# Kernel optimization log

Hardware: AMD Instinct MI355X
Metric: run time of the kernel (lower is better)

The kernel has to match this reference:

```python
import jax, jax.numpy as jnp
import numpy as np

D_MODEL = 1024
NUM_HEADS = 16
HEAD_DIM = D_MODEL // NUM_HEADS


def setup_inputs() -> dict:
    key = jax.random.key(0)
    ks = jax.random.split(key, 5)
    B, S, D_IN = 2, 2048, 1024
    x = jax.random.normal(ks[0], (B, S, D_IN), dtype=jnp.float32)
    std = 0.02
    wq = jax.random.normal(ks[1], (D_MODEL, D_IN), dtype=jnp.float32) * std
    wk = jax.random.normal(ks[2], (D_MODEL, D_IN), dtype=jnp.float32) * std
    wv = jax.random.normal(ks[3], (D_MODEL, D_IN), dtype=jnp.float32) * std
    wo = jax.random.normal(ks[4], (D_IN, D_MODEL), dtype=jnp.float32) * std
    return {"x": x, "wq": wq, "wk": wk, "wv": wv, "wo": wo}


def _mha(x, wq, wk, wv, wo):
    B, S, _ = x.shape
    H, Dh = NUM_HEADS, HEAD_DIM
    # projections: Linear applies x @ W.T with W of shape [out, in]
    q = (x @ wq.T).reshape(B, S, H, Dh).transpose(0, 2, 1, 3)  # [B,H,S,Dh]
    k = (x @ wk.T).reshape(B, S, H, Dh).transpose(0, 2, 1, 3)
    v = (x @ wv.T).reshape(B, S, H, Dh).transpose(0, 2, 1, 3)
    scores = jnp.einsum('bhqd,bhkd->bhqk', q, k) / jnp.sqrt(jnp.float32(Dh))
    causal = jnp.tril(jnp.ones((S, S), dtype=bool))  # True where attended
    scores = jnp.where(causal, scores, -jnp.inf)
    attn = jax.nn.softmax(scores, axis=-1)
    out = jnp.einsum('bhqk,bhkd->bhqd', attn, v)  # [B,H,S,Dh]
    out = out.transpose(0, 2, 1, 3).reshape(B, S, H * Dh)
    return out @ wo.T


def reference(x, wq, wk, wv, wo):
    return _mha(x, wq, wk, wv, wo)
```

## Files before the change

### kernel.cpp

```cpp
#include <hip/hip_runtime.h>
#include <hip/hip_bf16.h>
#include <stdint.h>

using bf16 = __hip_bfloat16;
typedef __attribute__((ext_vector_type(4))) short shorts4;
typedef __attribute__((ext_vector_type(8))) short short8;
typedef __attribute__((ext_vector_type(4))) float floatx4;
typedef __attribute__((ext_vector_type(16))) float floatx16;
typedef __attribute__((ext_vector_type(4))) unsigned int uintx4;

constexpr int BATCH = 2;
constexpr int SEQ   = 2048;
constexpr int NH    = 16;
constexpr int DH    = 64;
constexpr int DM    = 1024;
constexpr int MROWS = BATCH * SEQ;
constexpr int OUTN  = MROWS * DM;
constexpr int WN    = DM * DM;

__device__ inline short bfbits(float x) {
    bf16 h = __float2bfloat16(x);
    return __builtin_bit_cast(short, h);
}

__device__ inline unsigned pack2(float a, float b) {
    return (unsigned)(unsigned short)bfbits(a) |
           ((unsigned)(unsigned short)bfbits(b) << 16);
}

__device__ inline void async16(bf16* lds, const bf16* g) {
    __builtin_amdgcn_global_load_lds(
        (const __attribute__((address_space(1))) unsigned int*)g,
        (__attribute__((address_space(3))) unsigned int*)lds, 16, 0, 0);
}

__device__ inline void cvt8(const float* src, bf16* dst) {
    float4 f0 = *(const float4*)(src);
    float4 f1 = *(const float4*)(src + 4);
    short8 o;
    o[0] = bfbits(f0.x); o[1] = bfbits(f0.y); o[2] = bfbits(f0.z); o[3] = bfbits(f0.w);
    o[4] = bfbits(f1.x); o[5] = bfbits(f1.y); o[6] = bfbits(f1.z); o[7] = bfbits(f1.w);
    *(short8*)(dst) = o;
}

__global__ __launch_bounds__(256)
void cvt_all(const float* __restrict__ x,  const float* __restrict__ wq,
             const float* __restrict__ wk, const float* __restrict__ wv,
             const float* __restrict__ wo, bf16* __restrict__ dst,
             bf16* __restrict__ wob)
{
    const size_t i = ((size_t)blockIdx.x * 256 + threadIdx.x) * 8;
    if (i < (size_t)OUTN + 3 * WN) {
        const float* src; size_t off;
        if (i < (size_t)OUTN)               { src = x;  off = i; }
        else if (i < (size_t)OUTN + WN)     { src = wq; off = i - OUTN; }
        else if (i < (size_t)OUTN + 2 * WN) { src = wk; off = i - OUTN - WN; }
        else                                { src = wv; off = i - OUTN - 2 * (size_t)WN; }
        cvt8(src + off, dst + i);
    } else {
        const size_t off = i - OUTN - 3 * (size_t)WN;
        cvt8(wo + off, wob + off);
    }
}

__global__ __launch_bounds__(256)
void cvt_inputs(const float* __restrict__ x,  const float* __restrict__ wq,
                const float* __restrict__ wk, const float* __restrict__ wv,
                bf16* __restrict__ dst)
{
    const size_t i = ((size_t)blockIdx.x * 256 + threadIdx.x) * 8;
    const float* src; size_t off;
    if (i < (size_t)OUTN)               { src = x;  off = i; }
    else if (i < (size_t)OUTN + WN)     { src = wq; off = i - OUTN; }
    else if (i < (size_t)OUTN + 2 * WN) { src = wk; off = i - OUTN - WN; }
    else                                { src = wv; off = i - OUTN - 2 * (size_t)WN; }
    cvt8(src + off, dst + i);
}

__global__ __launch_bounds__(256)
void cvt_wo(const float* __restrict__ wo, bf16* __restrict__ dst)
{
    const size_t i = ((size_t)blockIdx.x * 256 + threadIdx.x) * 8;
    cvt8(wo + i, dst + i);
}

template<int MODE, int NZ>
__global__ __launch_bounds__(512, 2)
void gemm_mfma(const bf16* __restrict__ A,
               const bf16* __restrict__ W0, const bf16* __restrict__ W1,
               const bf16* __restrict__ W2,
               bf16* __restrict__ C0, bf16* __restrict__ C1, bf16* __restrict__ C2,
               float* __restrict__ F)
{
    __shared__ __align__(16) bf16 smem[(1 + NZ) * 8192 * 2];

    const int t    = threadIdx.x;
    const int wave = t >> 6;
    const int lane = t & 63;
    const int quad = lane >> 4;
    const int l16  = lane & 15;
    const int m0 = blockIdx.y * 128;
    const int n0 = blockIdx.x * 128;
    const int wr = (wave >> 2) * 64;
    const int wc = (wave & 3) * 32;

    const bf16* Wp[3] = {W0, W1, W2};

    floatx4 acc[NZ][4][2] = {};

    auto stage = [&](int kt, int bb) {
        bf16* Bb = smem + bb * (1 + NZ) * 8192;
        const int k0 = kt * 64;
        #pragma unroll
        for (int p = 0; p < 2; p++) {
            const int ck = p * 512 + t;
            const int kr = ck >> 3;
            const int kg = (ck & 7) ^ (kr & 7);
            async16(Bb + ck * 8, A + (size_t)(m0 + kr) * DM + k0 + kg * 8);
            #pragma unroll
            for (int zz = 0; zz < NZ; zz++)
                async16(Bb + (1 + zz) * 8192 + ck * 8,
                        Wp[zz] + (size_t)(n0 + kr) * DM + k0 + kg * 8);
        }
    };

    stage(0, 0);
    __syncthreads();

    for (int kt = 0; kt < DM / 64; ++kt) {
        const int cur = kt & 1;
        if (kt + 1 < DM / 64) stage(kt + 1, cur ^ 1);

        const bf16* Bb = smem + cur * (1 + NZ) * 8192;

        #pragma unroll
        for (int ks = 0; ks < 2; ks++) {
            short8 af[4];
            #pragma unroll
            for (int i = 0; i < 4; i++) {
                const int r = wr + i * 16 + l16;
                af[i] = *(const short8*)(Bb + r * 64 + ((ks * 4 + quad) ^ (r & 7)) * 8);
            }
            #pragma unroll
            for (int zz = 0; zz < NZ; zz++) {
                short8 wf[2];
                #pragma unroll
                for (int j = 0; j < 2; j++) {
                    const int n = wc + j * 16 + l16;
                    wf[j] = *(const short8*)(Bb + (1 + zz) * 8192 + n * 64 +
                                             ((ks * 4 + quad) ^ (n & 7)) * 8);
                }
                __builtin_amdgcn_s_setprio(1);
                #pragma unroll
                for (int i = 0; i < 4; i++)
                    #pragma unroll
                    for (int j = 0; j < 2; j++)
                        acc[zz][i][j] = __builtin_amdgcn_mfma_f32_16x16x32_bf16(
                            af[i], wf[j], acc[zz][i][j], 0, 0, 0);
                __builtin_amdgcn_s_setprio(0);
            }
        }
        __syncthreads();
    }

    #pragma unroll
    for (int zz = 0; zz < NZ; zz++) {
        #pragma unroll
        for (int i = 0; i < 4; i++) {
            #pragma unroll
            for (int j = 0; j < 2; j++) {
                if (MODE == 0 && zz == 2) {
                    const int s0 = m0 + wr + i * 16 + quad * 4;
                    const int gn = n0 + wc + j * 16 + l16;
                    const int b = s0 >> 11, sr = s0 & (SEQ - 1);
                    const int h = gn >> 6,  d = gn & (DH - 1);
                    shorts4 pv;
                    #pragma unroll
                    for (int r = 0; r < 4; r++) pv[r] = bfbits(acc[zz][i][j][r]);
                    *(shorts4*)(C2 + (((size_t)(b * NH + h)) * DH + d) * SEQ + sr) = pv;
                } else {
                    #pragma unroll
                    for (int r = 0; r < 4; r++) {
                        const int gm = m0 + wr + i * 16 + quad * 4 + r;
                        const int gn = n0 + wc + j * 16 + l16;
                        if (MODE == 1) {
                            F[(size_t)gm * DM + gn] = acc[zz][i][j][r];
                        } else {
                            float av = acc[zz][i][j][r];
                            if (zz == 0) av *= 0.18033688f;
                            bf16* dst = (zz == 0) ? C0 : C1;
                            dst[(size_t)gm * DM + gn] = __float2bfloat16(av);
                        }
                    }
                }
            }
        }
    }
}

__device__ __forceinline__ void attn_tile(const bf16* Ks, int kbase, int qrow,
                                          const short8 (&qf)[4],
                                          floatx16 (&oacc)[2], float& lsum,
                                          int khalf, int hi, int l32)
{
    if (kbase > qrow + 31) return;
    const bf16* Vs = Ks + 8192;
    const int qg = qrow + l32;

    #pragma unroll
    for (int kt = 0; kt < 2; kt++) {
        const int kb = kbase + kt * 32;
        if (kb > qrow + 31) continue;

        const int krow = khalf * 64 + kt * 32 + l32;
        floatx16 sc = {};
        #pragma unroll
        for (int sg = 0; sg < 4; sg++) {
            const int g = (sg * 2 + hi) ^ (krow & 7);
            short8 kf = *(const short8*)(Ks + krow * 64 + g * 8);
            sc = __builtin_amdgcn_mfma_f32_32x32x16_bf16(kf, qf[sg], sc, 0, 0, 0);
        }

        if (kb + 31 > qrow) {
            #pragma unroll
            for (int r = 0; r < 16; r++) {
                const int key = kb + (r & 3) + 8 * (r >> 2) + 4 * hi;
                sc[r] = (key <= qg) ? sc[r] : -1e30f;
            }
        }

        #pragma unroll
        for (int r = 0; r < 16; r++) {
            const float p = __builtin_amdgcn_exp2f(sc[r]);
            sc[r] = p;
            lsum += p;
        }

        unsigned d[4][2];
        #pragma unroll
        for (int g = 0; g < 4; g++) {
            d[g][0] = pack2(sc[4 * g + 0], sc[4 * g + 1]);
            d[g][1] = pack2(sc[4 * g + 2], sc[4 * g + 3]);
        }

        #pragma unroll
        for (int h16 = 0; h16 < 2; h16++) {
            const unsigned a0 = d[h16 * 2][0],     a1 = d[h16 * 2][1];
            const unsigned b0 = d[h16 * 2 + 1][0], b1 = d[h16 * 2 + 1][1];
            const unsigned mine0 = hi ? b0 : a0, mine1 = hi ? b1 : a1;
            const unsigned give0 = hi ? a0 : b0, give1 = hi ? a1 : b1;
            const unsigned r0 = (unsigned)__shfl_xor((int)give0, 32, 64);
            const unsigned r1 = (unsigned)__shfl_xor((int)give1, 32, 64);
            uintx4 pw;
            pw[0] = hi ? r0 : mine0;
            pw[1] = hi ? r1 : mine1;
            pw[2] = hi ? mine0 : r0;
            pw[3] = hi ? mine1 : r1;
            short8 pb = __builtin_bit_cast(short8, pw);

            const int Gbase = khalf * 8 + kt * 4 + h16 * 2 + hi;
            #pragma unroll
            for (int tile = 0; tile < 2; tile++) {
                const int vrow = tile * 32 + l32;
                const int vg = Gbase ^ (vrow & 15);
                short8 vf = *(const short8*)(Vs + vrow * 128 + vg * 8);
                oacc[tile] = __builtin_amdgcn_mfma_f32_32x32x16_bf16(vf, pb, oacc[tile], 0, 0, 0);
            }
        }
    }
}

__global__ __launch_bounds__(512, 2)
void attn_flash(bf16* __restrict__ Q, const bf16* __restrict__ K,
                const bf16* __restrict__ Vt)
{
    __shared__ __align__(16) bf16 smem[49152];

    const int t    = threadIdx.x;
    const int wave = t >> 6;
    const int lane = t & 63;
    const int hi   = lane >> 5;
    const int l32  = lane & 31;

    const int id  = blockIdx.x + 8 * (blockIdx.y + NH * blockIdx.z);
    const int xcd = id & 7;
    const int jj  = id >> 3;
    const int p   = xcd * 4 + (jj >> 3);
    const int h   = p & (NH - 1);
    const int b   = p >> 4;
    const int qtA = jj & 7;
    const int qtB = 15 - qtA;

    const int hc  = h * DH;
    const size_t rowb = (size_t)b * SEQ;
    const size_t bhv  = ((size_t)(b * NH + h)) * SEQ * DH;

    const int qw    = wave & 3;
    const int khalf = wave >> 2;
    const int qrA = qtA * 128 + qw * 32;
    const int qrB = qtB * 128 + qw * 32;

    short8 qfA[4], qfB[4];
    #pragma unroll
    for (int sg = 0; sg < 4; sg++) {
        qfA[sg] = *(const short8*)(Q + (rowb + qrA + l32) * DM + hc + sg * 16 + hi * 8);
        qfB[sg] = *(const short8*)(Q + (rowb + qrB + l32) * DM + hc + sg * 16 + hi * 8);
    }

    floatx16 oaccA[2] = {}, oaccB[2] = {};
    float lsumA = 0.f, lsumB = 0.f;

    constexpr int NSLOT = 17;

    auto slotK0 = [&](int s) { return (s <= qtA ? s : s - qtA - 1) * 128; };

    auto stage = [&](int s) {
        bf16* Kb = smem + (s % 3) * 16384;
        bf16* Vb = Kb + 8192;
        const int k0 = slotK0(s);
        #pragma unroll
        for (int pp = 0; pp < 2; pp++) {
            const int ck = pp * 512 + t;
            const int kr = ck >> 3;
            const int kg = (ck & 7) ^ (kr & 7);
            async16(Kb + ck * 8, K + (rowb + k0 + kr) * DM + hc + kg * 8);
            const int vr = ck >> 4;
            const int vg = (ck & 15) ^ (vr & 15);
            async16(Vb + ck * 8, Vt + bhv + (size_t)vr * SEQ + k0 + vg * 8);
        }
    };

    stage(0);
    stage(1);
    for (int s = 0; s < NSLOT - 1; ++s) {
        asm volatile("s_waitcnt vmcnt(4)" ::: "memory");
        __builtin_amdgcn_s_barrier();
        if (s + 2 < NSLOT) stage(s + 2);
        const bf16* Ks = smem + (s % 3) * 16384;
        if (s <= qtA)
            attn_tile(Ks, s * 128 + khalf * 64, qrA, qfA, oaccA, lsumA, khalf, hi, l32);
        else
            attn_tile(Ks, (s - qtA - 1) * 128 + khalf * 64, qrB, qfB, oaccB, lsumB, khalf, hi, l32);
    }
    asm volatile("s_waitcnt vmcnt(0)" ::: "memory");
    __builtin_amdgcn_s_barrier();
    attn_tile(smem + ((NSLOT - 1) % 3) * 16384,
              (NSLOT - 2 - qtA) * 128 + khalf * 64, qrB, qfB, oaccB, lsumB, khalf, hi, l32);

    lsumA += __shfl_xor(lsumA, 32, 64);
    lsumB += __shfl_xor(lsumB, 32, 64);

    __syncthreads();
    float* dmp = (float*)smem;
    float* lP  = dmp + 2 * 4 * 32 * 66;
    if (khalf == 1) {
        #pragma unroll
        for (int m = 0; m < 2; m++) {
            const floatx16* oc = m ? oaccB : oaccA;
            #pragma unroll
            for (int tile = 0; tile < 2; tile++)
                #pragma unroll
                for (int r = 0; r < 16; r++) {
                    const int dd = tile * 32 + (r & 3) + 8 * (r >> 2) + 4 * hi;
                    dmp[((m * 4 + qw) * 32 + l32) * 66 + dd] = oc[tile][r];
                }
            if (!hi) lP[(m * 4 + qw) * 32 + l32] = m ? lsumB : lsumA;
        }
    }
    __syncthreads();

    if (khalf == 0) {
        bf16* T8 = smem + 34304 + qw * 2304;
        #pragma unroll
        for (int m = 0; m < 2; m++) {
            const floatx16* oc = m ? oaccB : oaccA;
            const float lt = (m ? lsumB : lsumA) + lP[(m * 4 + qw) * 32 + l32];
            const float invl = 1.0f / lt;
            const int qrow = m ? qrB : qrA;
            #pragma unroll
            for (int tile = 0; tile < 2; tile++)
                #pragma unroll
                for (int rq = 0; rq < 4; rq++) {
                    shorts4 v4;
                    #pragma unroll
                    for (int sg = 0; sg < 4; sg++) {
                        const int r = rq * 4 + sg;
                        const int dd = tile * 32 + (r & 3) + 8 * (r >> 2) + 4 * hi;
                        const float comb = oc[tile][r] + dmp[((m * 4 + qw) * 32 + l32) * 66 + dd];
                        v4[sg] = bfbits(comb * invl);
                    }
                    *(shorts4*)(T8 + l32 * 72 + tile * 32 + rq * 8 + hi * 4) = v4;
                }
            asm volatile("s_waitcnt lgkmcnt(0)" ::: "memory");
            #pragma unroll
            for (int p2 = 0; p2 < 4; p2++) {
                const int rq = (lane >> 3) + p2 * 8;
                const int dd = (lane & 7) * 8;
                short8 v8 = *(const short8*)(T8 + rq * 72 + dd);
                *(short8*)(Q + (rowb + qrow + rq) * DM + hc + dd) = v8;
            }
            asm volatile("s_waitcnt lgkmcnt(0)" ::: "memory");
        }
    }
}

extern "C" void kernel_launch(void* const* d_in, const int* in_sizes, int n_in,
                              void* d_out, int out_size, void* d_ws, size_t ws_size,
                              hipStream_t stream)
{
    const float* x  = (const float*)d_in[0];
    const float* wq = (const float*)d_in[1];
    const float* wk = (const float*)d_in[2];
    const float* wv = (const float*)d_in[3];
    const float* wo = (const float*)d_in[4];
    float* out = (float*)d_out;

    bf16* qb = (bf16*)d_ws;
    bf16* kb = qb + (size_t)OUTN;
    bf16* vb = kb + (size_t)OUTN;

    bf16* xb  = (bf16*)d_out;
    bf16* wqb = xb + (size_t)OUTN;
    bf16* wkb = wqb + WN;
    bf16* wvb = wkb + WN;

    const bool wsBig = ws_size >= (size_t)(3 * (size_t)OUTN + WN) * sizeof(bf16);

    if (wsBig) {
        bf16* wob = vb + (size_t)OUTN;
        cvt_all<<<(OUTN + 4 * WN) / (8 * 256), 256, 0, stream>>>(
            x, wq, wk, wv, wo, xb, wob);
        gemm_mfma<0, 3><<<dim3(DM / 128, MROWS / 128), dim3(512), 0, stream>>>(
            xb, wqb, wkb, wvb, qb, kb, vb, nullptr);
        attn_flash<<<dim3(8, NH, BATCH), dim3(512), 0, stream>>>(qb, kb, vb);
        gemm_mfma<1, 1><<<dim3(DM / 128, MROWS / 128), dim3(512), 0, stream>>>(
            qb, wob, nullptr, nullptr, nullptr, nullptr, nullptr, out);
    } else {
        cvt_inputs<<<(OUTN + 3 * WN) / (8 * 256), 256, 0, stream>>>(x, wq, wk, wv, xb);
        gemm_mfma<0, 3><<<dim3(DM / 128, MROWS / 128), dim3(512), 0, stream>>>(
            xb, wqb, wkb, wvb, qb, kb, vb, nullptr);
        attn_flash<<<dim3(8, NH, BATCH), dim3(512), 0, stream>>>(qb, kb, vb);
        bf16* wob = kb;
        cvt_wo<<<WN / (8 * 256), 256, 0, stream>>>(wo, wob);
        gemm_mfma<1, 1><<<dim3(DM / 128, MROWS / 128), dim3(512), 0, stream>>>(
            qb, wob, nullptr, nullptr, nullptr, nullptr, nullptr, out);
    }
}
```

Measured before the change: 157.5 us.

## Split attention key tile across four waves per query group with 1024-thread blocks

The attention kernel now runs 16 waves per block instead of 8. Each query group of 32 rows is served by four waves, and each wave handles one 32-key quarter of the 128-key tile instead of a 64-key half. Staging issues one K and one V chunk per thread, and the final combine reduces partial outputs and row sums from four waves through shared memory in four sync-separated passes. This aims to raise wave-level parallelism and latency hiding during the MFMA and exp work, at the cost of more block barriers, a longer reduction epilogue, and tighter register and occupancy limits with 1024 threads.

Result: slower. 210.2 us (+33.5%).

```diff
diff --git a/kernel.cpp b/kernel.cpp
--- a/kernel.cpp
+++ b/kernel.cpp
@@ -198,79 +198,73 @@
     }
 }
 
-__device__ __forceinline__ void attn_tile(const bf16* Ks, int kbase, int qrow,
-                                          const short8 (&qf)[4],
-                                          floatx16 (&oacc)[2], float& lsum,
-                                          int khalf, int hi, int l32)
-{
-    if (kbase > qrow + 31) return;
+__device__ __forceinline__ void attn_kt(const bf16* Ks, int kb, int qrow,
+                                        const short8 (&qf)[4],
+                                        floatx16 (&oacc)[2], float& lsum,
+                                        int kq, int hi, int l32)
+{
+    if (kb > qrow + 31) return;
     const bf16* Vs = Ks + 8192;
     const int qg = qrow + l32;
-
-    #pragma unroll
-    for (int kt = 0; kt < 2; kt++) {
-        const int kb = kbase + kt * 32;
-        if (kb > qrow + 31) continue;
-
-        const int krow = khalf * 64 + kt * 32 + l32;
-        floatx16 sc = {};
-        #pragma unroll
-        for (int sg = 0; sg < 4; sg++) {
-            const int g = (sg * 2 + hi) ^ (krow & 7);
-            short8 kf = *(const short8*)(Ks + krow * 64 + g * 8);
-            sc = __builtin_amdgcn_mfma_f32_32x32x16_bf16(kf, qf[sg], sc, 0, 0, 0);
-        }
-
-        if (kb + 31 > qrow) {
-            #pragma unroll
-            for (int r = 0; r < 16; r++) {
-                const int key = kb + (r & 3) + 8 * (r >> 2) + 4 * hi;
-                sc[r] = (key <= qg) ? sc[r] : -1e30f;
-            }
-        }
-
+    const int krow = kq * 32 + l32;
+
+    floatx16 sc = {};
+    #pragma unroll
+    for (int sg = 0; sg < 4; sg++) {
+        const int g = (sg * 2 + hi) ^ (krow & 7);
+        short8 kf = *(const short8*)(Ks + krow * 64 + g * 8);
+        sc = __builtin_amdgcn_mfma_f32_32x32x16_bf16(kf, qf[sg], sc, 0, 0, 0);
+    }
+
+    if (kb + 31 > qrow) {
         #pragma unroll
         for (int r = 0; r < 16; r++) {
-            const float p = __builtin_amdgcn_exp2f(sc[r]);
-            sc[r] = p;
-            lsum += p;
-        }
-
-        unsigned d[4][2];
-        #pragma unroll
-        for (int g = 0; g < 4; g++) {
-            d[g][0] = pack2(sc[4 * g + 0], sc[4 * g + 1]);
-            d[g][1] = pack2(sc[4 * g + 2], sc[4 * g + 3]);
-        }
-
-        #pragma unroll
-        for (int h16 = 0; h16 < 2; h16++) {
-            const unsigned a0 = d[h16 * 2][0],     a1 = d[h16 * 2][1];
-            const unsigned b0 = d[h16 * 2 + 1][0], b1 = d[h16 * 2 + 1][1];
-            const unsigned mine0 = hi ? b0 : a0, mine1 = hi ? b1 : a1;
-            const unsigned give0 = hi ? a0 : b0, give1 = hi ? a1 : b1;
-            const unsigned r0 = (unsigned)__shfl_xor((int)give0, 32, 64);
-            const unsigned r1 = (unsigned)__shfl_xor((int)give1, 32, 64);
-            uintx4 pw;
-            pw[0] = hi ? r0 : mine0;
-            pw[1] = hi ? r1 : mine1;
-            pw[2] = hi ? mine0 : r0;
-            pw[3] = hi ? mine1 : r1;
-            short8 pb = __builtin_bit_cast(short8, pw);
-
-            const int Gbase = khalf * 8 + kt * 4 + h16 * 2 + hi;
-            #pragma unroll
-            for (int tile = 0; tile < 2; tile++) {
-                const int vrow = tile * 32 + l32;
-                const int vg = Gbase ^ (vrow & 15);
-                short8 vf = *(const short8*)(Vs + vrow * 128 + vg * 8);
-                oacc[tile] = __builtin_amdgcn_mfma_f32_32x32x16_bf16(vf, pb, oacc[tile], 0, 0, 0);
-            }
-        }
-    }
-}
-
-__global__ __launch_bounds__(512, 2)
+            const int key = kb + (r & 3) + 8 * (r >> 2) + 4 * hi;
+            sc[r] = (key <= qg) ? sc[r] : -1e30f;
+        }
+    }
+
+    #pragma unroll
+    for (int r = 0; r < 16; r++) {
+        const float p = __builtin_amdgcn_exp2f(sc[r]);
+        sc[r] = p;
+        lsum += p;
+    }
+
+    unsigned d[4][2];
+    #pragma unroll
+    for (int g = 0; g < 4; g++) {
+        d[g][0] = pack2(sc[4 * g + 0], sc[4 * g + 1]);
+        d[g][1] = pack2(sc[4 * g + 2], sc[4 * g + 3]);
+    }
+
+    #pragma unroll
+    for (int h16 = 0; h16 < 2; h16++) {
+        const unsigned a0 = d[h16 * 2][0],     a1 = d[h16 * 2][1];
+        const unsigned b0 = d[h16 * 2 + 1][0], b1 = d[h16 * 2 + 1][1];
+        const unsigned mine0 = hi ? b0 : a0, mine1 = hi ? b1 : a1;
+        const unsigned give0 = hi ? a0 : b0, give1 = hi ? a1 : b1;
+        const unsigned r0 = (unsigned)__shfl_xor((int)give0, 32, 64);
+        const unsigned r1 = (unsigned)__shfl_xor((int)give1, 32, 64);
+        uintx4 pw;
+        pw[0] = hi ? r0 : mine0;
+        pw[1] = hi ? r1 : mine1;
+        pw[2] = hi ? mine0 : r0;
+        pw[3] = hi ? mine1 : r1;
+        short8 pb = __builtin_bit_cast(short8, pw);
+
+        const int Gbase = kq * 4 + h16 * 2 + hi;
+        #pragma unroll
+        for (int tile = 0; tile < 2; tile++) {
+            const int vrow = tile * 32 + l32;
+            const int vg = Gbase ^ (vrow & 15);
+            short8 vf = *(const short8*)(Vs + vrow * 128 + vg * 8);
+            oacc[tile] = __builtin_amdgcn_mfma_f32_32x32x16_bf16(vf, pb, oacc[tile], 0, 0, 0);
+        }
+    }
+}
+
+__global__ __launch_bounds__(1024, 4)
 void attn_flash(bf16* __restrict__ Q, const bf16* __restrict__ K,
                 const bf16* __restrict__ Vt)
 {
@@ -295,8 +289,8 @@
     const size_t rowb = (size_t)b * SEQ;
     const size_t bhv  = ((size_t)(b * NH + h)) * SEQ * DH;
 
-    const int qw    = wave & 3;
-    const int khalf = wave >> 2;
+    const int qw = wave & 3;
+    const int kq = wave >> 2;
     const int qrA = qtA * 128 + qw * 32;
     const int qrB = qtB * 128 + qw * 32;
 
@@ -318,63 +312,74 @@
         bf16* Kb = smem + (s % 3) * 16384;
         bf16* Vb = Kb + 8192;
         const int k0 = slotK0(s);
-        #pragma unroll
-        for (int pp = 0; pp < 2; pp++) {
-            const int ck = pp * 512 + t;
-            const int kr = ck >> 3;
-            const int kg = (ck & 7) ^ (kr & 7);
-            async16(Kb + ck * 8, K + (rowb + k0 + kr) * DM + hc + kg * 8);
-            const int vr = ck >> 4;
-            const int vg = (ck & 15) ^ (vr & 15);
-            async16(Vb + ck * 8, Vt + bhv + (size_t)vr * SEQ + k0 + vg * 8);
-        }
+        const int kr = t >> 3;
+        const int kg = (t & 7) ^ (kr & 7);
+        async16(Kb + t * 8, K + (rowb + k0 + kr) * DM + hc + kg * 8);
+        const int vr = t >> 4;
+        const int vg = (t & 15) ^ (vr & 15);
+        async16(Vb + t * 8, Vt + bhv + (size_t)vr * SEQ + k0 + vg * 8);
     };
 
     stage(0);
     stage(1);
     for (int s = 0; s < NSLOT - 1; ++s) {
-        asm volatile("s_waitcnt vmcnt(4)" ::: "memory");
+        asm volatile("s_waitcnt vmcnt(2)" ::: "memory");
         __builtin_amdgcn_s_barrier();
         if (s + 2 < NSLOT) stage(s + 2);
         const bf16* Ks = smem + (s % 3) * 16384;
         if (s <= qtA)
-            attn_tile(Ks, s * 128 + khalf * 64, qrA, qfA, oaccA, lsumA, khalf, hi, l32);
+            attn_kt(Ks, s * 128 + kq * 32, qrA, qfA, oaccA, lsumA, kq, hi, l32);
         else
-            attn_tile(Ks, (s - qtA - 1) * 128 + khalf * 64, qrB, qfB, oaccB, lsumB, khalf, hi, l32);
+            attn_kt(Ks, (s - qtA - 1) * 128 + kq * 32, qrB, qfB, oaccB, lsumB, kq, hi, l32);
     }
     asm volatile("s_waitcnt vmcnt(0)" ::: "memory");
     __builtin_amdgcn_s_barrier();
-    attn_tile(smem + ((NSLOT - 1) % 3) * 16384,
-              (NSLOT - 2 - qtA) * 128 + khalf * 64, qrB, qfB, oaccB, lsumB, khalf, hi, l32);
+    attn_kt(smem + ((NSLOT - 1) % 3) * 16384,
+            (NSLOT - 2 - qtA) * 128 + kq * 32, qrB, qfB, oaccB, lsumB, kq, hi, l32);
 
     lsumA += __shfl_xor(lsumA, 32, 64);
     lsumB += __shfl_xor(lsumB, 32, 64);
 
     __syncthreads();
     float* dmp = (float*)smem;
-    float* lP  = dmp + 2 * 4 * 32 * 66;
-    if (khalf == 1) {
+    float* lP  = dmp + 13056;
+    if (!hi) {
+        lP[((0 * 4 + qw) * 4 + kq) * 32 + l32] = lsumA;
+        lP[((1 * 4 + qw) * 4 + kq) * 32 + l32] = lsumB;
+    }
+
+    #pragma unroll
+    for (int r4 = 0; r4 < 4; ++r4) {
+        const int m = r4 >> 1, tile = r4 & 1;
+        __syncthreads();
+        if (kq > 0) {
+            #pragma unroll
+            for (int r = 0; r < 16; r++) {
+                const int dim = (r & 3) + 8 * (r >> 2) + 4 * hi;
+                const float v = m ? oaccB[tile][r] : oaccA[tile][r];
+                dmp[((qw * 3 + (kq - 1)) * 32 + l32) * 34 + dim] = v;
+            }
+        }
+        __syncthreads();
+        if (kq == 0) {
+            #pragma unroll
+            for (int r = 0; r < 16; r++) {
+                const int dim = (r & 3) + 8 * (r >> 2) + 4 * hi;
+                const float v = dmp[((qw * 3 + 0) * 32 + l32) * 34 + dim]
+                              + dmp[((qw * 3 + 1) * 32 + l32) * 34 + dim]
+                              + dmp[((qw * 3 + 2) * 32 + l32) * 34 + dim];
+                if (m) oaccB[tile][r] += v; else oaccA[tile][r] += v;
+            }
+        }
+    }
+
+    if (kq == 0) {
+        bf16* T8 = smem + 28672 + qw * 2304;
         #pragma unroll
         for (int m = 0; m < 2; m++) {
-            const floatx16* oc = m ? oaccB : oaccA;
-            #pragma unroll
-            for (int tile = 0; tile < 2; tile++)
-                #pragma unroll
-                for (int r = 0; r < 16; r++) {
-                    const int dd = tile * 32 + (r & 3) + 8 * (r >> 2) + 4 * hi;
-                    dmp[((m * 4 + qw) * 32 + l32) * 66 + dd] = oc[tile][r];
-                }
-            if (!hi) lP[(m * 4 + qw) * 32 + l32] = m ? lsumB : lsumA;
-        }
-    }
-    __syncthreads();
-
-    if (khalf == 0) {
-        bf16* T8 = smem + 34304 + qw * 2304;
-        #pragma unroll
-        for (int m = 0; m < 2; m++) {
-            const floatx16* oc = m ? oaccB : oaccA;
-            const float lt = (m ? lsumB : lsumA) + lP[(m * 4 + qw) * 32 + l32];
+            float lt = 0.f;
+            #pragma unroll
+            for (int j = 0; j < 4; j++) lt += lP[((m * 4 + qw) * 4 + j) * 32 + l32];
             const float invl = 1.0f / lt;
             const int qrow = m ? qrB : qrA;
             #pragma unroll
@@ -385,9 +390,8 @@
                     #pragma unroll
                     for (int sg = 0; sg < 4; sg++) {
                         const int r = rq * 4 + sg;
-                        const int dd = tile * 32 + (r & 3) + 8 * (r >> 2) + 4 * hi;
-                        const float comb = oc[tile][r] + dmp[((m * 4 + qw) * 32 + l32) * 66 + dd];
-                        v4[sg] = bfbits(comb * invl);
+                        const float cv = m ? oaccB[tile][r] : oaccA[tile][r];
+                        v4[sg] = bfbits(cv * invl);
                     }
                     *(shorts4*)(T8 + l32 * 72 + tile * 32 + rq * 8 + hi * 4) = v4;
                 }
@@ -432,14 +436,14 @@
             x, wq, wk, wv, wo, xb, wob);
         gemm_mfma<0, 3><<<dim3(DM / 128, MROWS / 128), dim3(512), 0, stream>>>(
             xb, wqb, wkb, wvb, qb, kb, vb, nullptr);
-        attn_flash<<<dim3(8, NH, BATCH), dim3(512), 0, stream>>>(qb, kb, vb);
+        attn_flash<<<dim3(8, NH, BATCH), dim3(1024), 0, stream>>>(qb, kb, vb);
         gemm_mfma<1, 1><<<dim3(DM / 128, MROWS / 128), dim3(512), 0, stream>>>(
             qb, wob, nullptr, nullptr, nullptr, nullptr, nullptr, out);
     } else {
         cvt_inputs<<<(OUTN + 3 * WN) / (8 * 256), 256, 0, stream>>>(x, wq, wk, wv, xb);
         gemm_mfma<0, 3><<<dim3(DM / 128, MROWS / 128), dim3(512), 0, stream>>>(
             xb, wqb, wkb, wvb, qb, kb, vb, nullptr);
-        attn_flash<<<dim3(8, NH, BATCH), dim3(512), 0, stream>>>(qb, kb, vb);
+        attn_flash<<<dim3(8, NH, BATCH), dim3(1024), 0, stream>>>(qb, kb, vb);
         bf16* wob = kb;
         cvt_wo<<<WN / (8 * 256), 256, 0, stream>>>(wo, wob);
         gemm_mfma<1, 1><<<dim3(DM / 128, MROWS / 128), dim3(512), 0, stream>>>(
```

## Triple-buffer GEMM K-tiles with vmcnt waits and smaller BK for fused QKV

Applied to the files above, without the earlier changes.

Replaces the double-buffered K loop with a three-stage ring buffer. Two tiles are prefetched ahead, and the loop waits with s_waitcnt vmcnt on the older loads followed by a barrier, which drops the trailing __syncthreads. For the three-weight QKV variant the K tile shrinks from 64 to 32, so the triple buffer fits in LDS and occupancy is kept. Deeper prefetch should hide global-load latency better, at the cost of more barriers per K step for the QKV GEMM and a hand-counted vmcnt that must match the issued loads.

After: 161.1 us. 1.02x slower.

```diff
diff --git a/kernel.cpp b/kernel.cpp
--- a/kernel.cpp
+++ b/kernel.cpp
@@ -92,7 +92,17 @@
                bf16* __restrict__ C0, bf16* __restrict__ C1, bf16* __restrict__ C2,
                float* __restrict__ F)
 {
-    __shared__ __align__(16) bf16 smem[(1 + NZ) * 8192 * 2];
+    constexpr int BK   = (NZ == 3) ? 32 : 64;
+    constexpr int GR   = BK / 8;
+    constexpr int SWM  = GR - 1;
+    constexpr int TEN  = 1 + NZ;
+    constexpr int TB   = 128 * BK;
+    constexpr int RNDS = BK / 32;
+    constexpr int VM   = RNDS * TEN;
+    constexpr int NT   = DM / BK;
+    constexpr int LG   = (GR == 4) ? 2 : 3;
+
+    __shared__ __align__(16) bf16 smem[TEN * TB * 3];
 
     const int t    = threadIdx.x;
     const int wave = t >> 6;
@@ -108,38 +118,41 @@
 
     floatx4 acc[NZ][4][2] = {};
 
-    auto stage = [&](int kt, int bb) {
-        bf16* Bb = smem + bb * (1 + NZ) * 8192;
-        const int k0 = kt * 64;
-        #pragma unroll
-        for (int p = 0; p < 2; p++) {
+    auto stage = [&](int kt) {
+        bf16* Bb = smem + (kt % 3) * TEN * TB;
+        const int k0 = kt * BK;
+        #pragma unroll
+        for (int p = 0; p < RNDS; p++) {
             const int ck = p * 512 + t;
-            const int kr = ck >> 3;
-            const int kg = (ck & 7) ^ (kr & 7);
+            const int kr = ck >> LG;
+            const int kg = (ck & SWM) ^ (kr & SWM);
             async16(Bb + ck * 8, A + (size_t)(m0 + kr) * DM + k0 + kg * 8);
             #pragma unroll
             for (int zz = 0; zz < NZ; zz++)
-                async16(Bb + (1 + zz) * 8192 + ck * 8,
+                async16(Bb + (1 + zz) * TB + ck * 8,
                         Wp[zz] + (size_t)(n0 + kr) * DM + k0 + kg * 8);
         }
     };
 
-    stage(0, 0);
-    __syncthreads();
-
-    for (int kt = 0; kt < DM / 64; ++kt) {
-        const int cur = kt & 1;
-        if (kt + 1 < DM / 64) stage(kt + 1, cur ^ 1);
-
-        const bf16* Bb = smem + cur * (1 + NZ) * 8192;
-
-        #pragma unroll
-        for (int ks = 0; ks < 2; ks++) {
+    stage(0);
+    stage(1);
+
+    for (int kt = 0; kt < NT; ++kt) {
+        if (kt < NT - 1) asm volatile("s_waitcnt vmcnt(%0)" :: "i"(VM) : "memory");
+        else             asm volatile("s_waitcnt vmcnt(0)" ::: "memory");
+        __builtin_amdgcn_s_barrier();
+        if (kt + 2 < NT) stage(kt + 2);
+
+        const bf16* Bb = smem + (kt % 3) * TEN * TB;
+
+        #pragma unroll
+        for (int ks = 0; ks < BK / 32; ks++) {
             short8 af[4];
             #pragma unroll
             for (int i = 0; i < 4; i++) {
                 const int r = wr + i * 16 + l16;
-                af[i] = *(const short8*)(Bb + r * 64 + ((ks * 4 + quad) ^ (r & 7)) * 8);
+                const int g = (ks * 4 + quad) ^ (r & SWM);
+                af[i] = *(const short8*)(Bb + r * BK + g * 8);
             }
             #pragma unroll
             for (int zz = 0; zz < NZ; zz++) {
@@ -147,8 +160,8 @@
                 #pragma unroll
                 for (int j = 0; j < 2; j++) {
                     const int n = wc + j * 16 + l16;
-                    wf[j] = *(const short8*)(Bb + (1 + zz) * 8192 + n * 64 +
-                                             ((ks * 4 + quad) ^ (n & 7)) * 8);
+                    const int g = (ks * 4 + quad) ^ (n & SWM);
+                    wf[j] = *(const short8*)(Bb + (1 + zz) * TB + n * BK + g * 8);
                 }
                 __builtin_amdgcn_s_setprio(1);
                 #pragma unroll
@@ -160,7 +173,6 @@
                 __builtin_amdgcn_s_setprio(0);
             }
         }
-        __syncthreads();
     }
 
     #pragma unroll
```
